# Kernel optimization log

Measured on AMD Instinct MI355X. Metric: run time of the kernel, lower is better.

The kernel has to match this reference:

```python
import jax, jax.numpy as jnp
import numpy as np


def _hilbert_filter(S):
    # scipy.signal.hilbert analytic-signal spectrum multiplier
    h = np.zeros(S, dtype=np.float32)
    h[0] = 1.0
    if S % 2 == 0:
        h[S // 2] = 1.0
        h[1:S // 2] = 2.0
    else:
        h[1:(S + 1) // 2] = 2.0
    return h


def setup_inputs() -> dict:
    key = jax.random.key(0)
    B, C, S = 16, 64, 2048
    x = jax.random.normal(key, (B, C, S), dtype=jnp.float32)
    return {"x": x}


def reference(x) -> jnp.ndarray:
    B, C, S = x.shape
    h = jnp.asarray(_hilbert_filter(S))
    # Analytic signal via FFT (batched over all B*C channels at once,
    # instead of recomputing hilbert() per (i,j) pair as the torch loop does)
    analytic = jnp.fft.ifft(jnp.fft.fft(x, axis=-1) * h, axis=-1)  # [B,C,S] complex
    theta = jnp.angle(analytic)                                    # [B,C,S]
    # Pairwise instantaneous phase differences: [B,C,C,S]
    d = theta[:, :, None, :] - theta[:, None, :, :]
    # angle(exp(1j*d)) wraps d to (-pi,pi]; original zeroes exact +/-pi values.
    # sign(sin(d)) == sign(wrapped d) with +/-pi (and 0) mapped to 0 -- identical math.
    pli = jnp.abs(jnp.mean(jnp.sign(jnp.sin(d)), axis=-1))         # [B,C,C]
    # diagonal: d == 0 -> sign 0 -> mean 0, matching the skipped i==j entries
    return pli.astype(jnp.float32)
```

## Files before the change

### kernel.cpp

```cpp
#include <hip/hip_runtime.h>

#define Bv 16
#define Cv 64
#define Sv 2048
#define NSEG 64
#define SSEG 32
#define ROWS 68

__device__ __forceinline__ void bf_f(float2& u, float2& v, const float2 w) {
    const float dr = u.x - v.x, di = u.y - v.y;
    u.x += v.x; u.y += v.y;
    v.x = dr * w.x - di * w.y;
    v.y = dr * w.y + di * w.x;
}
__device__ __forceinline__ void bf_i(float2& u, float2& v, const float2 w) {
    const float vr = v.x * w.x + v.y * w.y;
    const float vi = v.y * w.x - v.x * w.y;
    v.x = u.x - vr; v.y = u.y - vi;
    u.x += vr; u.y += vi;
}

__global__ __launch_bounds__(256) void hilbert_kernel(const float* __restrict__ x,
                                                      float* __restrict__ y) {
    __shared__ float2 zz[Sv];
    __shared__ float2 Wt[Sv];
    const int t = threadIdx.x;
    const int c0 = blockIdx.x * 2;
    const float* x0 = x + (size_t)c0 * Sv;
    const float* x1 = x0 + Sv;

    for (int k = t; k < Sv; k += 256) {
        if (k == 0) { Wt[0] = make_float2(1.0f, 0.0f); continue; }
        const int half = 1 << (31 - __clz(k));
        const int pos = k - half;
        float sn, cs;
        sincosf(-3.14159265358979323846f * (float)pos / (float)half, &sn, &cs);
        Wt[k] = make_float2(cs, sn);
    }

    float2 z[8];
    #pragma unroll
    for (int k = 0; k < 8; ++k)
        z[k] = make_float2(x0[t + 256 * k], x1[t + 256 * k]);
    __syncthreads();

    #pragma unroll
    for (int k = 0; k < 4; ++k) bf_f(z[k], z[k + 4], Wt[1024 + t + 256 * k]);
    {
        const float2 wA = Wt[512 + t], wB = Wt[512 + t + 256];
        bf_f(z[0], z[2], wA); bf_f(z[1], z[3], wB);
        bf_f(z[4], z[6], wA); bf_f(z[5], z[7], wB);
        const float2 wc = Wt[256 + t];
        bf_f(z[0], z[1], wc); bf_f(z[2], z[3], wc);
        bf_f(z[4], z[5], wc); bf_f(z[6], z[7], wc);
    }
    #pragma unroll
    for (int k = 0; k < 8; ++k) zz[t + 256 * k] = z[k];
    __syncthreads();

    {
        const int r = t & 31, base = (t >> 5) * 256 + r;
        #pragma unroll
        for (int k = 0; k < 8; ++k) z[k] = zz[base + 32 * k];
        #pragma unroll
        for (int k = 0; k < 4; ++k) bf_f(z[k], z[k + 4], Wt[128 + r + 32 * k]);
        const float2 wA = Wt[64 + r], wB = Wt[64 + r + 32];
        bf_f(z[0], z[2], wA); bf_f(z[1], z[3], wB);
        bf_f(z[4], z[6], wA); bf_f(z[5], z[7], wB);
        const float2 wc = Wt[32 + r];
        bf_f(z[0], z[1], wc); bf_f(z[2], z[3], wc);
        bf_f(z[4], z[5], wc); bf_f(z[6], z[7], wc);
        #pragma unroll
        for (int k = 0; k < 8; ++k) zz[base + 32 * k] = z[k];
    }
    __syncthreads();

    {
        const int r = t & 7, base0 = (t >> 3) * 32 + r, base1 = base0 + 1024;
        #pragma unroll
        for (int k = 0; k < 4; ++k) { z[k] = zz[base0 + 8 * k]; z[4 + k] = zz[base1 + 8 * k]; }
        const float2 wA = Wt[16 + r], wB = Wt[16 + r + 8];
        bf_f(z[0], z[2], wA); bf_f(z[1], z[3], wB);
        bf_f(z[4], z[6], wA); bf_f(z[5], z[7], wB);
        const float2 wc = Wt[8 + r];
        bf_f(z[0], z[1], wc); bf_f(z[2], z[3], wc);
        bf_f(z[4], z[5], wc); bf_f(z[6], z[7], wc);
        #pragma unroll
        for (int k = 0; k < 4; ++k) { zz[base0 + 8 * k] = z[k]; zz[base1 + 8 * k] = z[4 + k]; }
    }
    __syncthreads();

    {
        const int base = 8 * t;
        #pragma unroll
        for (int k = 0; k < 8; ++k) z[k] = zz[base + k];
        const float cq = 0.70710678118654752f;
        const float2 W1  = make_float2(1.0f, 0.0f);
        const float2 W41 = make_float2(cq, -cq);
        const float2 W42 = make_float2(0.0f, -1.0f);
        const float2 W43 = make_float2(-cq, -cq);
        bf_f(z[0], z[4], W1);  bf_f(z[1], z[5], W41);
        bf_f(z[2], z[6], W42); bf_f(z[3], z[7], W43);
        bf_f(z[0], z[2], W1); bf_f(z[1], z[3], W42);
        bf_f(z[4], z[6], W1); bf_f(z[5], z[7], W42);
        bf_f(z[0], z[1], W1); bf_f(z[2], z[3], W1);
        bf_f(z[4], z[5], W1); bf_f(z[6], z[7], W1);
        const float inv = 1.0f / (float)Sv;
        #pragma unroll
        for (int k = 0; k < 8; ++k) {
            const int kk = (int)(__brev((unsigned)(base + k)) >> 21);
            const float m = (kk == 0 || kk == Sv / 2) ? inv : (kk < Sv / 2 ? 2.0f * inv : 0.0f);
            z[k].x *= m; z[k].y *= m;
        }
        bf_i(z[0], z[1], W1); bf_i(z[2], z[3], W1);
        bf_i(z[4], z[5], W1); bf_i(z[6], z[7], W1);
        bf_i(z[0], z[2], W1); bf_i(z[1], z[3], W42);
        bf_i(z[4], z[6], W1); bf_i(z[5], z[7], W42);
        bf_i(z[0], z[4], W1);  bf_i(z[1], z[5], W41);
        bf_i(z[2], z[6], W42); bf_i(z[3], z[7], W43);
        #pragma unroll
        for (int k = 0; k < 8; ++k) zz[base + k] = z[k];
    }
    __syncthreads();

    {
        const int r = t & 7, base0 = (t >> 3) * 32 + r, base1 = base0 + 1024;
        #pragma unroll
        for (int k = 0; k < 4; ++k) { z[k] = zz[base0 + 8 * k]; z[4 + k] = zz[base1 + 8 * k]; }
        const float2 wc = Wt[8 + r];
        bf_i(z[0], z[1], wc); bf_i(z[2], z[3], wc);
        bf_i(z[4], z[5], wc); bf_i(z[6], z[7], wc);
        const float2 wA = Wt[16 + r], wB = Wt[16 + r + 8];
        bf_i(z[0], z[2], wA); bf_i(z[1], z[3], wB);
        bf_i(z[4], z[6], wA); bf_i(z[5], z[7], wB);
        #pragma unroll
        for (int k = 0; k < 4; ++k) { zz[base0 + 8 * k] = z[k]; zz[base1 + 8 * k] = z[4 + k]; }
    }
    __syncthreads();

    {
        const int r = t & 31, base = (t >> 5) * 256 + r;
        #pragma unroll
        for (int k = 0; k < 8; ++k) z[k] = zz[base + 32 * k];
        const float2 wc = Wt[32 + r];
        bf_i(z[0], z[1], wc); bf_i(z[2], z[3], wc);
        bf_i(z[4], z[5], wc); bf_i(z[6], z[7], wc);
        const float2 wA = Wt[64 + r], wB = Wt[64 + r + 32];
        bf_i(z[0], z[2], wA); bf_i(z[1], z[3], wB);
        bf_i(z[4], z[6], wA); bf_i(z[5], z[7], wB);
        #pragma unroll
        for (int k = 0; k < 4; ++k) bf_i(z[k], z[k + 4], Wt[128 + r + 32 * k]);
        #pragma unroll
        for (int k = 0; k < 8; ++k) zz[base + 32 * k] = z[k];
    }
    __syncthreads();

    {
        #pragma unroll
        for (int k = 0; k < 8; ++k) z[k] = zz[t + 256 * k];
        const float2 wc = Wt[256 + t];
        bf_i(z[0], z[1], wc); bf_i(z[2], z[3], wc);
        bf_i(z[4], z[5], wc); bf_i(z[6], z[7], wc);
        const float2 wA = Wt[512 + t], wB = Wt[512 + t + 256];
        bf_i(z[0], z[2], wA); bf_i(z[1], z[3], wB);
        bf_i(z[4], z[6], wA); bf_i(z[5], z[7], wB);
        #pragma unroll
        for (int k = 0; k < 4; ++k) bf_i(z[k], z[k + 4], Wt[1024 + t + 256 * k]);
        float* y0 = y + (size_t)c0 * Sv;
        float* y1 = y0 + Sv;
        #pragma unroll
        for (int k = 0; k < 8; ++k) {
            const int n = t + 256 * k;
            y0[n] = z[k].y - x1[n];
            y1[n] = x0[n] - z[k].x;
        }
    }
}

__global__ __launch_bounds__(256) void pli_count_kernel(const float* __restrict__ x,
                                                        const float* __restrict__ y,
                                                        unsigned int* __restrict__ part) {
    __shared__ __align__(16) float xL[SSEG * ROWS];
    __shared__ __align__(16) float yL[SSEG * ROWS];
    const int blk = blockIdx.x;
    const int seg = blk & (NSEG - 1);
    const int b = blk >> 6;
    const int t = threadIdx.x;
    const float* xb = x + (size_t)b * Cv * Sv + seg * SSEG;
    const float* yb = y + (size_t)b * Cv * Sv + seg * SSEG;

    for (int e = t; e < Cv * SSEG; e += 256) {
        const int ch = e >> 5;
        const int s = e & (SSEG - 1);
        xL[s * ROWS + ch] = xb[(size_t)ch * Sv + s];
        yL[s * ROWS + ch] = yb[(size_t)ch * Sv + s];
    }
    __syncthreads();

    const int ti = t >> 4, tj = t & 15;
    const int i0 = ti * 4, j0 = tj * 4;
    int neg[4][4] = {};

    #pragma unroll 4
    for (int s = 0; s < SSEG; ++s) {
        const float4 xi = *(const float4*)&xL[s * ROWS + i0];
        const float4 yi = *(const float4*)&yL[s * ROWS + i0];
        const float4 xj = *(const float4*)&xL[s * ROWS + j0];
        const float4 yj = *(const float4*)&yL[s * ROWS + j0];
        const float xia[4] = {xi.x, xi.y, xi.z, xi.w};
        const float yia[4] = {yi.x, yi.y, yi.z, yi.w};
        const float xja[4] = {xj.x, xj.y, xj.z, xj.w};
        const float yja[4] = {yj.x, yj.y, yj.z, yj.w};
        #pragma unroll
        for (int a = 0; a < 4; ++a) {
            #pragma unroll
            for (int c = 0; c < 4; ++c) {
                const float cr = fmaf(yia[a], xja[c], -(xia[a] * yja[c]));
                neg[a][c] += (int)(__float_as_uint(cr) >> 31);
            }
        }
    }

    unsigned int* Pb = part + (size_t)(b * NSEG + seg) * (Cv * Cv / 4);
    #pragma unroll
    for (int a = 0; a < 4; ++a) {
        const unsigned int p = (unsigned)neg[a][0] | ((unsigned)neg[a][1] << 8)
                             | ((unsigned)neg[a][2] << 16) | ((unsigned)neg[a][3] << 24);
        Pb[(i0 + a) * (Cv / 4) + tj] = p;
    }
}

__global__ __launch_bounds__(256) void finalize_kernel(const unsigned int* __restrict__ part,
                                                       float* __restrict__ out) {
    const int idx = blockIdx.x * 256 + threadIdx.x;
    const int b = idx >> 12;
    const int ij = idx & 4095;
    const int i = ij >> 6, j = ij & 63;
    const unsigned int* p = part + (size_t)b * NSEG * 1024 + i * 16 + (j >> 2);
    const int sh = 8 * (j & 3);
    int negsum = 0;
    #pragma unroll 8
    for (int s = 0; s < NSEG; ++s)
        negsum += (int)((p[s * 1024] >> sh) & 0xFFu);
    out[idx] = (i == j) ? 0.0f
                        : fabsf((float)Sv - 2.0f * (float)negsum) * (1.0f / (float)Sv);
}

extern "C" void kernel_launch(void* const* d_in, const int* in_sizes, int n_in,
                              void* d_out, int out_size, void* d_ws, size_t ws_size,
                              hipStream_t stream) {
    const float* x = (const float*)d_in[0];
    float* y = (float*)d_ws;
    unsigned int* part = (unsigned int*)((char*)d_ws + (size_t)Bv * Cv * Sv * sizeof(float));
    float* out = (float*)d_out;

    hipLaunchKernelGGL(hilbert_kernel, dim3(Bv * Cv / 2), dim3(256), 0, stream, x, y);
    hipLaunchKernelGGL(pli_count_kernel, dim3(Bv * NSEG), dim3(256), 0, stream, x, y, part);
    hipLaunchKernelGGL(finalize_kernel, dim3(Bv * Cv * Cv / 256), dim3(256), 0, stream, part, out);
}
```

Before: 85.53 us.

## Compute FFT twiddles in registers and use 8x8 register tiles for PLI counting

The Hilbert FFT kernel drops the 2048-entry shared twiddle table, which needed 2048 sincosf calls per block. Each thread now computes three base twiddles and derives the rest by complex squaring and multiplication by fixed rotations. The PLI count kernel moves from 4x4 to 8x8 channel tiles per thread, with 4 lanes splitting the sample segment and merging counts through xor-shuffles. This cuts shared-memory loads per cross product but raises register pressure, and the squared twiddles lose a little precision.

```diff
diff --git a/kernel.cpp b/kernel.cpp
--- a/kernel.cpp
+++ b/kernel.cpp
@@ -19,40 +19,48 @@
     v.x = u.x - vr; v.y = u.y - vi;
     u.x += vr; u.y += vi;
 }
+__device__ __forceinline__ float2 csq(const float2 a) {
+    return make_float2(a.x * a.x - a.y * a.y, 2.0f * a.x * a.y);
+}
+__device__ __forceinline__ float2 cm1(const float2 a) {
+    const float cq = 0.70710678118654752f;
+    return make_float2(cq * (a.x + a.y), cq * (a.y - a.x));
+}
+__device__ __forceinline__ float2 cmi(const float2 a) {
+    return make_float2(a.y, -a.x);
+}
 
 __global__ __launch_bounds__(256) void hilbert_kernel(const float* __restrict__ x,
                                                       float* __restrict__ y) {
     __shared__ float2 zz[Sv];
-    __shared__ float2 Wt[Sv];
     const int t = threadIdx.x;
     const int c0 = blockIdx.x * 2;
     const float* x0 = x + (size_t)c0 * Sv;
     const float* x1 = x0 + Sv;
 
-    for (int k = t; k < Sv; k += 256) {
-        if (k == 0) { Wt[0] = make_float2(1.0f, 0.0f); continue; }
-        const int half = 1 << (31 - __clz(k));
-        const int pos = k - half;
-        float sn, cs;
-        sincosf(-3.14159265358979323846f * (float)pos / (float)half, &sn, &cs);
-        Wt[k] = make_float2(cs, sn);
-    }
+    const float PI = 3.14159265358979323846f;
+    float2 bA4, bB4, bC2;
+    sincosf(-PI * (float)t * (1.0f / 1024.0f), &bA4.y, &bA4.x);
+    sincosf(-PI * (float)(t & 31) * (1.0f / 128.0f), &bB4.y, &bB4.x);
+    sincosf(-PI * (float)(t & 7) * (1.0f / 16.0f), &bC2.y, &bC2.x);
+    const float2 bA2 = csq(bA4), bA1 = csq(bA2);
+    const float2 bB2 = csq(bB4), bB1 = csq(bB2);
+    const float2 bC1 = csq(bC2);
 
     float2 z[8];
     #pragma unroll
     for (int k = 0; k < 8; ++k)
         z[k] = make_float2(x0[t + 256 * k], x1[t + 256 * k]);
-    __syncthreads();
-
-    #pragma unroll
-    for (int k = 0; k < 4; ++k) bf_f(z[k], z[k + 4], Wt[1024 + t + 256 * k]);
-    {
-        const float2 wA = Wt[512 + t], wB = Wt[512 + t + 256];
-        bf_f(z[0], z[2], wA); bf_f(z[1], z[3], wB);
-        bf_f(z[4], z[6], wA); bf_f(z[5], z[7], wB);
-        const float2 wc = Wt[256 + t];
-        bf_f(z[0], z[1], wc); bf_f(z[2], z[3], wc);
-        bf_f(z[4], z[5], wc); bf_f(z[6], z[7], wc);
+
+    {
+        const float2 w1 = cm1(bA4);
+        bf_f(z[0], z[4], bA4);      bf_f(z[1], z[5], w1);
+        bf_f(z[2], z[6], cmi(bA4)); bf_f(z[3], z[7], cmi(w1));
+        const float2 wB = cmi(bA2);
+        bf_f(z[0], z[2], bA2); bf_f(z[1], z[3], wB);
+        bf_f(z[4], z[6], bA2); bf_f(z[5], z[7], wB);
+        bf_f(z[0], z[1], bA1); bf_f(z[2], z[3], bA1);
+        bf_f(z[4], z[5], bA1); bf_f(z[6], z[7], bA1);
     }
     #pragma unroll
     for (int k = 0; k < 8; ++k) zz[t + 256 * k] = z[k];
@@ -62,14 +70,14 @@
         const int r = t & 31, base = (t >> 5) * 256 + r;
         #pragma unroll
         for (int k = 0; k < 8; ++k) z[k] = zz[base + 32 * k];
-        #pragma unroll
-        for (int k = 0; k < 4; ++k) bf_f(z[k], z[k + 4], Wt[128 + r + 32 * k]);
-        const float2 wA = Wt[64 + r], wB = Wt[64 + r + 32];
-        bf_f(z[0], z[2], wA); bf_f(z[1], z[3], wB);
-        bf_f(z[4], z[6], wA); bf_f(z[5], z[7], wB);
-        const float2 wc = Wt[32 + r];
-        bf_f(z[0], z[1], wc); bf_f(z[2], z[3], wc);
-        bf_f(z[4], z[5], wc); bf_f(z[6], z[7], wc);
+        const float2 w1 = cm1(bB4);
+        bf_f(z[0], z[4], bB4);      bf_f(z[1], z[5], w1);
+        bf_f(z[2], z[6], cmi(bB4)); bf_f(z[3], z[7], cmi(w1));
+        const float2 wB = cmi(bB2);
+        bf_f(z[0], z[2], bB2); bf_f(z[1], z[3], wB);
+        bf_f(z[4], z[6], bB2); bf_f(z[5], z[7], wB);
+        bf_f(z[0], z[1], bB1); bf_f(z[2], z[3], bB1);
+        bf_f(z[4], z[5], bB1); bf_f(z[6], z[7], bB1);
         #pragma unroll
         for (int k = 0; k < 8; ++k) zz[base + 32 * k] = z[k];
     }
@@ -79,12 +87,11 @@
         const int r = t & 7, base0 = (t >> 3) * 32 + r, base1 = base0 + 1024;
         #pragma unroll
         for (int k = 0; k < 4; ++k) { z[k] = zz[base0 + 8 * k]; z[4 + k] = zz[base1 + 8 * k]; }
-        const float2 wA = Wt[16 + r], wB = Wt[16 + r + 8];
-        bf_f(z[0], z[2], wA); bf_f(z[1], z[3], wB);
-        bf_f(z[4], z[6], wA); bf_f(z[5], z[7], wB);
-        const float2 wc = Wt[8 + r];
-        bf_f(z[0], z[1], wc); bf_f(z[2], z[3], wc);
-        bf_f(z[4], z[5], wc); bf_f(z[6], z[7], wc);
+        const float2 wB = cmi(bC2);
+        bf_f(z[0], z[2], bC2); bf_f(z[1], z[3], wB);
+        bf_f(z[4], z[6], bC2); bf_f(z[5], z[7], wB);
+        bf_f(z[0], z[1], bC1); bf_f(z[2], z[3], bC1);
+        bf_f(z[4], z[5], bC1); bf_f(z[6], z[7], bC1);
         #pragma unroll
         for (int k = 0; k < 4; ++k) { zz[base0 + 8 * k] = z[k]; zz[base1 + 8 * k] = z[4 + k]; }
     }
@@ -127,12 +134,11 @@
         const int r = t & 7, base0 = (t >> 3) * 32 + r, base1 = base0 + 1024;
         #pragma unroll
         for (int k = 0; k < 4; ++k) { z[k] = zz[base0 + 8 * k]; z[4 + k] = zz[base1 + 8 * k]; }
-        const float2 wc = Wt[8 + r];
-        bf_i(z[0], z[1], wc); bf_i(z[2], z[3], wc);
-        bf_i(z[4], z[5], wc); bf_i(z[6], z[7], wc);
-        const float2 wA = Wt[16 + r], wB = Wt[16 + r + 8];
-        bf_i(z[0], z[2], wA); bf_i(z[1], z[3], wB);
-        bf_i(z[4], z[6], wA); bf_i(z[5], z[7], wB);
+        bf_i(z[0], z[1], bC1); bf_i(z[2], z[3], bC1);
+        bf_i(z[4], z[5], bC1); bf_i(z[6], z[7], bC1);
+        const float2 wB = cmi(bC2);
+        bf_i(z[0], z[2], bC2); bf_i(z[1], z[3], wB);
+        bf_i(z[4], z[6], bC2); bf_i(z[5], z[7], wB);
         #pragma unroll
         for (int k = 0; k < 4; ++k) { zz[base0 + 8 * k] = z[k]; zz[base1 + 8 * k] = z[4 + k]; }
     }
@@ -142,14 +148,14 @@
         const int r = t & 31, base = (t >> 5) * 256 + r;
         #pragma unroll
         for (int k = 0; k < 8; ++k) z[k] = zz[base + 32 * k];
-        const float2 wc = Wt[32 + r];
-        bf_i(z[0], z[1], wc); bf_i(z[2], z[3], wc);
-        bf_i(z[4], z[5], wc); bf_i(z[6], z[7], wc);
-        const float2 wA = Wt[64 + r], wB = Wt[64 + r + 32];
-        bf_i(z[0], z[2], wA); bf_i(z[1], z[3], wB);
-        bf_i(z[4], z[6], wA); bf_i(z[5], z[7], wB);
-        #pragma unroll
-        for (int k = 0; k < 4; ++k) bf_i(z[k], z[k + 4], Wt[128 + r + 32 * k]);
+        bf_i(z[0], z[1], bB1); bf_i(z[2], z[3], bB1);
+        bf_i(z[4], z[5], bB1); bf_i(z[6], z[7], bB1);
+        const float2 wB = cmi(bB2);
+        bf_i(z[0], z[2], bB2); bf_i(z[1], z[3], wB);
+        bf_i(z[4], z[6], bB2); bf_i(z[5], z[7], wB);
+        const float2 w1 = cm1(bB4);
+        bf_i(z[0], z[4], bB4);      bf_i(z[1], z[5], w1);
+        bf_i(z[2], z[6], cmi(bB4)); bf_i(z[3], z[7], cmi(w1));
         #pragma unroll
         for (int k = 0; k < 8; ++k) zz[base + 32 * k] = z[k];
     }
@@ -158,14 +164,14 @@
     {
         #pragma unroll
         for (int k = 0; k < 8; ++k) z[k] = zz[t + 256 * k];
-        const float2 wc = Wt[256 + t];
-        bf_i(z[0], z[1], wc); bf_i(z[2], z[3], wc);
-        bf_i(z[4], z[5], wc); bf_i(z[6], z[7], wc);
-        const float2 wA = Wt[512 + t], wB = Wt[512 + t + 256];
-        bf_i(z[0], z[2], wA); bf_i(z[1], z[3], wB);
-        bf_i(z[4], z[6], wA); bf_i(z[5], z[7], wB);
-        #pragma unroll
-        for (int k = 0; k < 4; ++k) bf_i(z[k], z[k + 4], Wt[1024 + t + 256 * k]);
+        bf_i(z[0], z[1], bA1); bf_i(z[2], z[3], bA1);
+        bf_i(z[4], z[5], bA1); bf_i(z[6], z[7], bA1);
+        const float2 wB = cmi(bA2);
+        bf_i(z[0], z[2], bA2); bf_i(z[1], z[3], wB);
+        bf_i(z[4], z[6], bA2); bf_i(z[5], z[7], wB);
+        const float2 w1 = cm1(bA4);
+        bf_i(z[0], z[4], bA4);      bf_i(z[1], z[5], w1);
+        bf_i(z[2], z[6], cmi(bA4)); bf_i(z[3], z[7], cmi(w1));
         float* y0 = y + (size_t)c0 * Sv;
         float* y1 = y0 + Sv;
         #pragma unroll
@@ -197,36 +203,55 @@
     }
     __syncthreads();
 
-    const int ti = t >> 4, tj = t & 15;
-    const int i0 = ti * 4, j0 = tj * 4;
-    int neg[4][4] = {};
-
-    #pragma unroll 4
-    for (int s = 0; s < SSEG; ++s) {
-        const float4 xi = *(const float4*)&xL[s * ROWS + i0];
-        const float4 yi = *(const float4*)&yL[s * ROWS + i0];
-        const float4 xj = *(const float4*)&xL[s * ROWS + j0];
-        const float4 yj = *(const float4*)&yL[s * ROWS + j0];
-        const float xia[4] = {xi.x, xi.y, xi.z, xi.w};
-        const float yia[4] = {yi.x, yi.y, yi.z, yi.w};
-        const float xja[4] = {xj.x, xj.y, xj.z, xj.w};
-        const float yja[4] = {yj.x, yj.y, yj.z, yj.w};
-        #pragma unroll
-        for (int a = 0; a < 4; ++a) {
+    const int sl = t & 3;
+    const int tpos = t >> 2;
+    const int ti = tpos >> 3, tj = tpos & 7;
+    const int i0 = ti * 8, j0 = tj * 8;
+    int neg[8][8] = {};
+
+    #pragma unroll 2
+    for (int q = 0; q < 8; ++q) {
+        const int s = sl + 4 * q;
+        float xi[8], yi[8], xj[8], yj[8];
+        *(float4*)&xi[0] = *(const float4*)&xL[s * ROWS + i0];
+        *(float4*)&xi[4] = *(const float4*)&xL[s * ROWS + i0 + 4];
+        *(float4*)&yi[0] = *(const float4*)&yL[s * ROWS + i0];
+        *(float4*)&yi[4] = *(const float4*)&yL[s * ROWS + i0 + 4];
+        *(float4*)&xj[0] = *(const float4*)&xL[s * ROWS + j0];
+        *(float4*)&xj[4] = *(const float4*)&xL[s * ROWS + j0 + 4];
+        *(float4*)&yj[0] = *(const float4*)&yL[s * ROWS + j0];
+        *(float4*)&yj[4] = *(const float4*)&yL[s * ROWS + j0 + 4];
+        #pragma unroll
+        for (int a = 0; a < 8; ++a) {
             #pragma unroll
-            for (int c = 0; c < 4; ++c) {
-                const float cr = fmaf(yia[a], xja[c], -(xia[a] * yja[c]));
+            for (int c = 0; c < 8; ++c) {
+                const float cr = fmaf(yi[a], xj[c], -(xi[a] * yj[c]));
                 neg[a][c] += (int)(__float_as_uint(cr) >> 31);
             }
         }
     }
 
-    unsigned int* Pb = part + (size_t)(b * NSEG + seg) * (Cv * Cv / 4);
     #pragma unroll
-    for (int a = 0; a < 4; ++a) {
-        const unsigned int p = (unsigned)neg[a][0] | ((unsigned)neg[a][1] << 8)
-                             | ((unsigned)neg[a][2] << 16) | ((unsigned)neg[a][3] << 24);
-        Pb[(i0 + a) * (Cv / 4) + tj] = p;
+    for (int a = 0; a < 8; ++a) {
+        #pragma unroll
+        for (int c = 0; c < 8; ++c) {
+            int v = neg[a][c];
+            v += __shfl_xor(v, 1);
+            v += __shfl_xor(v, 2);
+            neg[a][c] = v;
+        }
+    }
+
+    if (sl == 0) {
+        unsigned int* Pb = part + (size_t)blk * (Cv * Cv / 4);
+        #pragma unroll
+        for (int a = 0; a < 8; ++a) {
+            const unsigned int p0 = (unsigned)neg[a][0] | ((unsigned)neg[a][1] << 8)
+                                  | ((unsigned)neg[a][2] << 16) | ((unsigned)neg[a][3] << 24);
+            const unsigned int p1 = (unsigned)neg[a][4] | ((unsigned)neg[a][5] << 8)
+                                  | ((unsigned)neg[a][6] << 16) | ((unsigned)neg[a][7] << 24);
+            *(uint2*)&Pb[(i0 + a) * (Cv / 4) + 2 * tj] = make_uint2(p0, p1);
+        }
     }
 }
 
```

Result: slower. 101.4 us (+18.6%).
